# Optimization experiments

Measured on AMD Instinct MI355X. Metric: run time of the kernel, lower is better.

The kernel has to match this reference:

```python
import jax, jax.numpy as jnp
import numpy as np

B = 64
E = 512          # latent_size / h_dim
H = 8            # num_heads
D = E // H       # head_dim
MAX_AGENTS = 254 # max(agents_per_sample) for the deterministic counts below
NEG = -1e9


def setup_inputs() -> dict:
    key = jax.random.key(0)
    k_x, k_wi, k_bi, k_wo, k_bo = jax.random.split(key, 5)
    # deterministic variable agent counts in [128, 254]; sum == 11531, max == 254
    agents = jnp.array([128 + (3 * i) % 129 for i in range(B)], dtype=jnp.int32)
    total = 11531
    att_in = jax.random.normal(k_x, (total, E), dtype=jnp.float32)
    # nn.MultiheadAttention params: packed in-proj [3E, E] + bias, out-proj [E, E] + bias
    w_in = jax.random.normal(k_wi, (3 * E, E), dtype=jnp.float32) * 0.02
    b_in = jax.random.normal(k_bi, (3 * E,), dtype=jnp.float32) * 0.02
    w_out = jax.random.normal(k_wo, (E, E), dtype=jnp.float32) * 0.02
    b_out = jax.random.normal(k_bo, (E,), dtype=jnp.float32) * 0.02
    return {"att_in": att_in, "w_in": w_in, "b_in": b_in,
            "w_out": w_out, "b_out": b_out, "agents_per_sample": agents}


def reference(att_in, w_in, b_in, w_out, b_out, agents_per_sample):
    S = MAX_AGENTS
    # scatter packed rows into padded [B, S, E] via a clipped gather (jit-safe)
    offsets = jnp.cumsum(agents_per_sample) - agents_per_sample      # [B]
    pos = jnp.arange(S, dtype=jnp.int32)
    mask = pos[None, :] < agents_per_sample[:, None]                 # [B, S] valid
    idx = jnp.clip(offsets[:, None] + pos[None, :], 0, att_in.shape[0] - 1)
    padded = jnp.where(mask[..., None], att_in[idx], 0.0)            # [B, S, E]

    # fused QKV projection (torch packed in_proj), dropout disabled (eval)
    qkv = padded @ w_in.T + b_in                                     # [B, S, 3E]
    q, k, v = jnp.split(qkv, 3, axis=-1)
    q = q.reshape(B, S, H, D)
    k = k.reshape(B, S, H, D)
    v = v.reshape(B, S, H, D)

    scores = jnp.einsum('bqhd,bkhd->bhqk', q, k) * (D ** -0.5)      # [B, H, S, S]
    scores = jnp.where(mask[:, None, None, :], scores, NEG)          # key_padding_mask
    attn = jax.nn.softmax(scores, axis=-1)
    ctx = jnp.einsum('bhqk,bkhd->bqhd', attn, v).reshape(B, S, E)
    out = ctx @ w_out.T + b_out                                      # [B, S, E]
    # torch returns only valid rows per sample; zero the padded rows instead
    return out * mask[..., None]
```

## Files before the change

kernel.cpp:

```cpp
#include <hip/hip_runtime.h>
#include <hip/hip_bf16.h>

typedef __attribute__((ext_vector_type(8))) short bf16x8;
typedef __attribute__((ext_vector_type(4))) float f32x4;
typedef __attribute__((ext_vector_type(4))) int i32x4;
typedef __attribute__((ext_vector_type(4))) unsigned short u16x4;
typedef __attribute__((ext_vector_type(2))) unsigned ui2;
typedef __attribute__((ext_vector_type(4))) float fl4;

struct __attribute__((packed)) u16x4u { u16x4 v; };

__device__ __forceinline__ f32x4 mfma16(bf16x8 a, bf16x8 b, f32x4 c) {
    return __builtin_amdgcn_mfma_f32_16x16x32_bf16(a, b, c, 0, 0, 0);
}

__device__ __forceinline__ unsigned short f2b(float f) {
    unsigned u = __float_as_uint(f);
    unsigned r = (u + 0x7FFF + ((u >> 16) & 1)) >> 16;
    return (unsigned short)r;
}

__device__ __forceinline__ int bsearch_off(const int* s_off, int m) {
    int lo = 0, hi = 63;
    while (lo < hi) {
        int mid = (lo + hi + 1) >> 1;
        if (s_off[mid] <= m) lo = mid; else hi = mid - 1;
    }
    return lo;
}

__device__ __forceinline__ void gld_lds16(const __hip_bfloat16* g, __hip_bfloat16* l) {
    __builtin_amdgcn_global_load_lds(
        (const __attribute__((address_space(1))) void*)g,
        (__attribute__((address_space(3))) void*)l,
        16, 0, 0);
}

__global__ void k_prep(const unsigned short* __restrict__ src,
                       const void* __restrict__ b_in, const void* __restrict__ b_out,
                       const int* __restrict__ agents,
                       int* __restrict__ flag, int* __restrict__ offs,
                       float* __restrict__ bfi, float* __restrict__ bfo) {
    __shared__ int sh[256];
    __shared__ int sa[64];
    __shared__ int sflag;
    int tid = threadIdx.x;
    int h = 0;
    for (int i = tid; i < 16384; i += 256) {
        unsigned e = (src[i] >> 7) & 0xFF;
        if (e == 0xFF) h = 1;
    }
    sh[tid] = h;
    if (tid < 64) sa[tid] = agents[tid];
    __syncthreads();
    if (tid < 64) {
        int v = sh[tid] | sh[tid + 64] | sh[tid + 128] | sh[tid + 192];
        unsigned long long m = __ballot(v != 0);
        if (tid == 0) { flag[0] = (m != 0) ? 1 : 0; sflag = (m != 0) ? 1 : 0; }
        int ex = 0;
        for (int i = 0; i < 64; ++i) { int w = sa[i]; if (i < tid) ex += w; }
        offs[tid] = ex;
        if (tid == 63) offs[64] = ex + sa[63];
    }
    __syncthreads();
    int f = sflag;
    for (int i = tid; i < 1536; i += 256)
        bfi[i] = f ? ((const float*)b_in)[i]
                   : __bfloat162float(((const __hip_bfloat16*)b_in)[i]);
    for (int i = tid; i < 512; i += 256)
        bfo[i] = f ? ((const float*)b_out)[i]
                   : __bfloat162float(((const __hip_bfloat16*)b_out)[i]);
}

__global__ void k_cast_all(const void* __restrict__ sA, unsigned short* __restrict__ dA, int nA,
                           const void* __restrict__ sWi, unsigned short* __restrict__ dWi, int nWi,
                           const void* __restrict__ sWo, unsigned short* __restrict__ dWo, int nWo,
                           const int* __restrict__ flag) {
    int i = (blockIdx.x * 256 + threadIdx.x) * 4;
    const void* src; unsigned short* dst; int k;
    if (i < nA)            { src = sA;  dst = dA;  k = i; }
    else if (i < nA + nWi) { src = sWi; dst = dWi; k = i - nA; }
    else if (i < nA + nWi + nWo) { src = sWo; dst = dWo; k = i - nA - nWi; }
    else return;
    u16x4 o;
    if (flag[0]) {
        fl4 v = *(const fl4*)((const float*)src + k);
        o[0] = f2b(v[0]); o[1] = f2b(v[1]); o[2] = f2b(v[2]); o[3] = f2b(v[3]);
    } else {
        o = *(const u16x4*)((const unsigned short*)src + k);
    }
    *(u16x4*)(dst + k) = o;
}

template<int LDA, bool MROWS>
__device__ __forceinline__ void gemm_core(
    const __hip_bfloat16* __restrict__ A,
    const __hip_bfloat16* __restrict__ W,
    int m0, int n0, int total,
    __hip_bfloat16* As, __hip_bfloat16* Ws,
    f32x4 acc[4][2], int tid)
{
    int lane = tid & 63, quad = lane >> 4, c = lane & 15;
    int wave = tid >> 6;
    int wm = wave >> 2, wn = wave & 3;

    const __hip_bfloat16* gA[2];
    const __hip_bfloat16* gW[2];
    __hip_bfloat16* lA[2];
    __hip_bfloat16* lW[2];
#pragma unroll
    for (int j = 0; j < 2; ++j) {
        int L = j * 512 + tid;
        int row = L >> 3;
        int gseg = (L & 7) ^ (row & 7);
        int ar = m0 + row; if (ar > total - 1) ar = total - 1;
        gA[j] = A + (size_t)ar * LDA + gseg * 8;
        gW[j] = W + (size_t)(n0 + row) * 512 + gseg * 8;
        lA[j] = As + (size_t)(j * 512 + wave * 64) * 8;
        lW[j] = Ws + (size_t)(j * 512 + wave * 64) * 8;
    }

#pragma unroll
    for (int j = 0; j < 2; ++j) gld_lds16(gA[j], lA[j]);
#pragma unroll
    for (int j = 0; j < 2; ++j) gld_lds16(gW[j], lW[j]);

#pragma unroll
    for (int s = 0; s < 8; ++s) {
        const int cur = s & 1;
        const int nxt = cur ^ 1;
        if (s < 7) {
            int k0 = (s + 1) * 64;
#pragma unroll
            for (int j = 0; j < 2; ++j) gld_lds16(gA[j] + k0, lA[j] + nxt * (128 * 64));
#pragma unroll
            for (int j = 0; j < 2; ++j) gld_lds16(gW[j] + k0, lW[j] + nxt * (128 * 64));
            asm volatile("s_waitcnt vmcnt(4)" ::: "memory");
        } else {
            asm volatile("s_waitcnt vmcnt(0)" ::: "memory");
        }
        __builtin_amdgcn_s_barrier();
        const __hip_bfloat16* Ab = As + cur * (128 * 64);
        const __hip_bfloat16* Wb = Ws + cur * (128 * 64);
#pragma unroll
        for (int h = 0; h < 2; ++h) {
            bf16x8 af[4], wf[2];
            int ks = quad + 4 * h;
#pragma unroll
            for (int t = 0; t < 4; ++t) {
                int rowa = wm * 64 + t * 16 + c;
                af[t] = *(const bf16x8*)(Ab + (size_t)rowa * 64 + ((ks ^ (rowa & 7)) * 8));
            }
#pragma unroll
            for (int t = 0; t < 2; ++t) {
                int rowb = wn * 32 + t * 16 + c;
                wf[t] = *(const bf16x8*)(Wb + (size_t)rowb * 64 + ((ks ^ (rowb & 7)) * 8));
            }
#pragma unroll
            for (int i = 0; i < 4; ++i)
#pragma unroll
                for (int j = 0; j < 2; ++j)
                    acc[i][j] = MROWS ? mfma16(af[i], wf[j], acc[i][j])
                                      : mfma16(wf[j], af[i], acc[i][j]);
        }
        if (s < 7) __builtin_amdgcn_s_barrier();
    }
}

__global__ __launch_bounds__(512, 4) void k_qkv(
    const __hip_bfloat16* __restrict__ A,
    const __hip_bfloat16* __restrict__ W,
    const float* __restrict__ bias,
    const int* __restrict__ offs,
    __hip_bfloat16* __restrict__ qP,
    __hip_bfloat16* __restrict__ kP,
    __hip_bfloat16* __restrict__ vT,
    int total, int MT)
{
    __shared__ __hip_bfloat16 As[2 * 128 * 64];
    __shared__ __hip_bfloat16 Ws[2 * 128 * 64];
    __shared__ int s_off[65];
    int l = blockIdx.x;
    int inner = l >> 3;
    int cb = inner % 12;
    int rb = (l & 7) + 8 * (inner / 12);
    if (rb >= MT) return;
    int n0 = cb * 128;
    int m0 = rb * 128;
    int tid = threadIdx.x;
    if (tid < 65) s_off[tid] = offs[tid];
    int lane = tid & 63, quad = lane >> 4, c = lane & 15;
    int wave = tid >> 6, wm = wave >> 2, wn = wave & 3;
    f32x4 z = {0.f, 0.f, 0.f, 0.f};
    f32x4 acc[4][2] = {{z,z},{z,z},{z,z},{z,z}};

    if (n0 < 1024) {
        gemm_core<512, false>(A, W, m0, n0, total, As, Ws, acc, tid);
        __hip_bfloat16* dst = (n0 < 512) ? qP : kP;
        int nb = n0 & 511;
        int head = (nb + wn * 32) >> 6;
        int cb32 = (wn & 1) * 32;
        fl4 bv4[2];
#pragma unroll
        for (int j = 0; j < 2; ++j)
            bv4[j] = *(const fl4*)&bias[n0 + wn * 32 + j * 16 + quad * 4];
#pragma unroll
        for (int i = 0; i < 4; ++i) {
            int m = m0 + wm * 64 + i * 16 + c;
            if (m >= total) continue;
            int lo = bsearch_off(s_off, m);
            int vs = m - s_off[lo];
            size_t rowp = ((size_t)(lo * 8 + head) * 256 + vs) * 64;
#pragma unroll
            for (int j = 0; j < 2; ++j) {
                int dcol = cb32 + j * 16 + quad * 4;
                u16x4 o;
#pragma unroll
                for (int r = 0; r < 4; ++r) o[r] = f2b(acc[i][j][r] + bv4[j][r]);
                *(u16x4*)&dst[rowp + dcol] = o;
            }
        }
    } else {
        gemm_core<512, true>(A, W, m0, n0, total, As, Ws, acc, tid);
        float bv[2];
#pragma unroll
        for (int j = 0; j < 2; ++j) bv[j] = bias[n0 + wn * 32 + j * 16 + c];
#pragma unroll
        for (int i = 0; i < 4; ++i) {
            int m_base = m0 + wm * 64 + i * 16 + quad * 4;
            if (m_base >= total) continue;
            int lo = bsearch_off(s_off, m_base);
            bool vec = (m_base + 3 < total) && (s_off[lo + 1] > m_base + 3);
            if (vec) {
                int vs = m_base - s_off[lo];
#pragma unroll
                for (int j = 0; j < 2; ++j) {
                    int vc = n0 - 1024 + wn * 32 + j * 16 + c;
                    size_t idx = ((size_t)(lo * 8 + (vc >> 6)) * 64 + (vc & 63)) * 256 + vs;
                    u16x4 o;
#pragma unroll
                    for (int r = 0; r < 4; ++r) o[r] = f2b(acc[i][j][r] + bv[j]);
                    ((u16x4u*)&vT[idx])->v = o;
                }
            } else {
#pragma unroll
                for (int r = 0; r < 4; ++r) {
                    int m = m_base + r;
                    if (m >= total) continue;
                    int lo2 = bsearch_off(s_off, m);
                    int vs2 = m - s_off[lo2];
#pragma unroll
                    for (int j = 0; j < 2; ++j) {
                        int vc = n0 - 1024 + wn * 32 + j * 16 + c;
                        vT[((size_t)(lo2 * 8 + (vc >> 6)) * 64 + (vc & 63)) * 256 + vs2] =
                            __float2bfloat16(acc[i][j][r] + bv[j]);
                    }
                }
            }
        }
    }
}

__global__ __launch_bounds__(256, 2) void k_attn(
    const __hip_bfloat16* __restrict__ qP,
    const __hip_bfloat16* __restrict__ kP,
    const __hip_bfloat16* __restrict__ vT,
    __hip_bfloat16* __restrict__ ctx,
    const int* __restrict__ agents,
    const int* __restrict__ offs)
{
    __shared__ __attribute__((aligned(16))) char Pl[4][16 * 80];
    int bh = blockIdx.x;
    int b = bh >> 3, h = bh & 7;
    int n = agents[b];
    int off = offs[b];
    int qtiles = (n + 15) >> 4;
    int stmax = (qtiles + 1) >> 1;
    int tid = threadIdx.x;
    int wave = tid >> 6, lane = tid & 63, quad = lane >> 4, c = lane & 15;
    const __hip_bfloat16* qbase = qP + (size_t)bh * 256 * 64;
    const __hip_bfloat16* kbase = kP + (size_t)bh * 256 * 64 + quad * 8;
    const __hip_bfloat16* vbase = vT + (size_t)bh * 64 * 256;
    char* Plw = &Pl[wave][0];

    bf16x8 qB[4][2];
    int nt = 0;
#pragma unroll
    for (int t = 0; t < 4; ++t) {
        int qt = wave + 4 * t;
        if (qt < qtiles) {
            nt = t + 1;
            int qr = qt * 16 + c; if (qr > n - 1) qr = n - 1;
            const __hip_bfloat16* qp = qbase + (size_t)qr * 64 + quad * 8;
            qB[t][0] = *(const bf16x8*)qp;
            qB[t][1] = *(const bf16x8*)(qp + 32);
        }
    }

    f32x4 z = {0.f, 0.f, 0.f, 0.f};
    f32x4 O[4][4] = {{z,z,z,z},{z,z,z,z},{z,z,z,z},{z,z,z,z}};
    float sm[4] = {0.f, 0.f, 0.f, 0.f};

    auto LK = [&](int st, bf16x8 kA[2][2], bf16x8 vA[4]) {
        int k0 = st * 32;
#pragma unroll
        for (int ti = 0; ti < 2; ++ti) {
            int kr = k0 + ti * 16 + c; if (kr > n - 1) kr = n - 1;
            const __hip_bfloat16* kp = kbase + (size_t)kr * 64;
            kA[ti][0] = *(const bf16x8*)kp;
            kA[ti][1] = *(const bf16x8*)(kp + 32);
        }
#pragma unroll
        for (int dt = 0; dt < 4; ++dt)
            vA[dt] = *(const bf16x8*)(vbase + (size_t)(dt * 16 + c) * 256 + k0 + quad * 8);
    };

    auto CMP = [&](int st, bf16x8 kA[2][2], bf16x8 vA[4]) {
        int k0 = st * 32;
#pragma unroll
        for (int t = 0; t < 4; ++t) {
            if (t < nt) {
#pragma unroll
                for (int ti = 0; ti < 2; ++ti) {
                    f32x4 s = mfma16(kA[ti][0], qB[t][0], z);
                    s = mfma16(kA[ti][1], qB[t][1], s);
                    int kbase_i = k0 + ti * 16 + quad * 4;
                    float p0 = (kbase_i + 0 < n) ? __expf(s[0] * 0.125f) : 0.f;
                    float p1 = (kbase_i + 1 < n) ? __expf(s[1] * 0.125f) : 0.f;
                    float p2 = (kbase_i + 2 < n) ? __expf(s[2] * 0.125f) : 0.f;
                    float p3 = (kbase_i + 3 < n) ? __expf(s[3] * 0.125f) : 0.f;
                    sm[t] += (p0 + p1) + (p2 + p3);
                    ui2 dw;
                    dw[0] = (unsigned)f2b(p0) | ((unsigned)f2b(p1) << 16);
                    dw[1] = (unsigned)f2b(p2) | ((unsigned)f2b(p3) << 16);
                    *(ui2*)(Plw + c * 80 + ti * 32 + quad * 8) = dw;
                }
                bf16x8 pB = *(const bf16x8*)(Plw + c * 80 + quad * 16);
#pragma unroll
                for (int dt = 0; dt < 4; ++dt)
                    O[t][dt] = mfma16(vA[dt], pB, O[t][dt]);
            }
        }
    };

    bf16x8 kA[2][2], vA[4], kB[2][2], vB[4], kC[2][2], vC[4];
    LK(0, kA, vA);
    if (1 < stmax) LK(1, kB, vB);
    for (int st = 0; st < stmax; st += 3) {
        if (st + 2 < stmax) LK(st + 2, kC, vC);
        CMP(st, kA, vA);
        if (st + 3 < stmax) LK(st + 3, kA, vA);
        if (st + 1 < stmax) CMP(st + 1, kB, vB);
        if (st + 4 < stmax) LK(st + 4, kB, vB);
        if (st + 2 < stmax) CMP(st + 2, kC, vC);
    }

#pragma unroll
    for (int t = 0; t < 4; ++t) {
        if (t < nt) {
            float v = sm[t];
            v += __shfl_xor(v, 16);
            v += __shfl_xor(v, 32);
            float iv = 1.0f / v;
            int q = (wave + 4 * t) * 16 + c;
            if (q < n) {
                size_t row = (size_t)(off + q) * 512 + h * 64;
#pragma unroll
                for (int dt = 0; dt < 4; ++dt) {
                    u16x4 o;
#pragma unroll
                    for (int r = 0; r < 4; ++r) o[r] = f2b(O[t][dt][r] * iv);
                    *(u16x4*)&ctx[row + dt * 16 + quad * 4] = o;
                }
            }
        }
    }
}

__global__ __launch_bounds__(512, 4) void k_out(
    const __hip_bfloat16* __restrict__ A,
    const __hip_bfloat16* __restrict__ W,
    const float* __restrict__ bias,
    const int* __restrict__ offs,
    const int* __restrict__ agents,
    void* __restrict__ out,
    const int* __restrict__ flag,
    int total, int MT)
{
    __shared__ __hip_bfloat16 As[2 * 128 * 64];
    __shared__ __hip_bfloat16 Ws[2 * 128 * 64];
    __shared__ int s_off[65];
    int l = blockIdx.x;
    int MTpad = ((MT + 7) >> 3) << 3;
    int tid = threadIdx.x;
    if (l >= 4 * MTpad) {
        int b = l - 4 * MTpad;
        int n = agents[b];
        int esz = flag[0] ? 4 : 2;
        long long base = ((long long)b * 254 + n) * 512 * esz;
        long long bytes = (long long)(254 - n) * 512 * esz;
        for (long long i = (long long)tid * 16; i < bytes; i += (long long)512 * 16)
            *(i32x4*)((char*)out + base + i) = (i32x4){0, 0, 0, 0};
        return;
    }
    int inner = l >> 3;
    int cb = inner & 3;
    int rb = (l & 7) + 8 * (inner >> 2);
    if (rb >= MT) return;
    int n0 = cb * 128;
    int m0 = rb * 128;
    if (tid < 65) s_off[tid] = offs[tid];
    f32x4 z = {0.f, 0.f, 0.f, 0.f};
    f32x4 acc[4][2] = {{z,z},{z,z},{z,z},{z,z}};
    gemm_core<512, false>(A, W, m0, n0, total, As, Ws, acc, tid);

    int f32m = flag[0];
    int lane = tid & 63, quad = lane >> 4, c = lane & 15;
    int wave = tid >> 6, wm = wave >> 2, wn = wave & 3;
    fl4 bv4[2];
#pragma unroll
    for (int j = 0; j < 2; ++j)
        bv4[j] = *(const fl4*)&bias[n0 + wn * 32 + j * 16 + quad * 4];
#pragma unroll
    for (int i = 0; i < 4; ++i) {
        int m = m0 + wm * 64 + i * 16 + c;
        if (m >= total) continue;
        int lo = bsearch_off(s_off, m);
        int os_ = m - s_off[lo];
        size_t rowb = ((size_t)(lo * 254 + os_)) * 512;
#pragma unroll
        for (int j = 0; j < 2; ++j) {
            int col0 = n0 + wn * 32 + j * 16 + quad * 4;
            if (f32m) {
                fl4 o;
#pragma unroll
                for (int r = 0; r < 4; ++r) o[r] = acc[i][j][r] + bv4[j][r];
                *(fl4*)&((float*)out)[rowb + col0] = o;
            } else {
                u16x4 o;
#pragma unroll
                for (int r = 0; r < 4; ++r) o[r] = f2b(acc[i][j][r] + bv4[j][r]);
                *(u16x4*)&((__hip_bfloat16*)out)[rowb + col0] = o;
            }
        }
    }
}

extern "C" void kernel_launch(void* const* d_in, const int* in_sizes, int n_in,
                              void* d_out, int out_size, void* d_ws, size_t ws_size,
                              hipStream_t stream) {
    const void* att_in = d_in[0];
    const void* w_in   = d_in[1];
    const void* b_in   = d_in[2];
    const void* w_out  = d_in[3];
    const void* b_out  = d_in[4];
    const int* agents  = (const int*)d_in[5];
    int total = in_sizes[0] / 512;

    char* p = (char*)d_ws;
    int* flag  = (int*)p;                 p += 256;
    int* offs  = (int*)p;                 p += 512;
    float* bfi = (float*)p;               p += 1536 * 4;
    float* bfo = (float*)p;               p += 512 * 4;
    __hip_bfloat16* WinBf  = (__hip_bfloat16*)p;  p += (size_t)1536 * 512 * 2;
    __hip_bfloat16* WoutBf = (__hip_bfloat16*)p;  p += (size_t)512 * 512 * 2;
    __hip_bfloat16* Abf    = (__hip_bfloat16*)p;  p += (size_t)total * 512 * 2;
    __hip_bfloat16* qP     = (__hip_bfloat16*)p;  p += (size_t)512 * 256 * 64 * 2;
    __hip_bfloat16* kP     = (__hip_bfloat16*)p;  p += (size_t)512 * 256 * 64 * 2;
    __hip_bfloat16* vT     = (__hip_bfloat16*)p;  p += (size_t)512 * 64 * 256 * 2;
    __hip_bfloat16* ctx    = (__hip_bfloat16*)p;  p += (size_t)total * 512 * 2;

    int nA = total * 512, nWi = 1536 * 512, nWo = 512 * 512;
    int ntot = nA + nWi + nWo;

    k_prep<<<1, 256, 0, stream>>>((const unsigned short*)att_in, b_in, b_out,
                                  agents, flag, offs, bfi, bfo);
    k_cast_all<<<(ntot / 4 + 255) / 256, 256, 0, stream>>>(
        att_in, (unsigned short*)Abf, nA,
        w_in,   (unsigned short*)WinBf, nWi,
        w_out,  (unsigned short*)WoutBf, nWo, flag);

    int MT = (total + 127) / 128;
    int MTpad = ((MT + 7) / 8) * 8;
    k_qkv<<<12 * MTpad, 512, 0, stream>>>(Abf, WinBf, bfi, offs, qP, kP, vT, total, MT);
    k_attn<<<512, 256, 0, stream>>>(qP, kP, vT, ctx, agents, offs);
    k_out<<<4 * MTpad + 64, 512, 0, stream>>>(ctx, WoutBf, bfo, offs, agents,
                                              d_out, flag, total, MT);
}
```

Before: 173.4 us.

## Triple-buffer A tiles in GEMM core and reuse LDS for segment offsets

The shared GEMM core now keeps three LDS buffers for A tiles and two for W tiles, so A loads are issued two k-steps ahead and more global loads stay in flight, with the waitcnt thresholds changed to match. The offsets table no longer has its own shared array. It is loaded into the A buffer after the GEMM, behind extra barriers. The extra 16 KB of A buffer raises LDS use per block and may reduce how many blocks fit on a CU.

Measured after the change: 175.1 us. About the same (+1.0%).

```diff
diff --git a/kernel.cpp b/kernel.cpp
--- a/kernel.cpp
+++ b/kernel.cpp
@@ -97,7 +97,8 @@
     const __hip_bfloat16* __restrict__ A,
     const __hip_bfloat16* __restrict__ W,
     int m0, int n0, int total,
-    __hip_bfloat16* As, __hip_bfloat16* Ws,
+    __hip_bfloat16* As,
+    __hip_bfloat16* Ws,
     f32x4 acc[4][2], int tid)
 {
     int lane = tid & 63, quad = lane >> 4, c = lane & 15;
@@ -124,24 +125,32 @@
     for (int j = 0; j < 2; ++j) gld_lds16(gA[j], lA[j]);
 #pragma unroll
     for (int j = 0; j < 2; ++j) gld_lds16(gW[j], lW[j]);
+#pragma unroll
+    for (int j = 0; j < 2; ++j) gld_lds16(gA[j] + 64, lA[j] + 8192);
 
 #pragma unroll
     for (int s = 0; s < 8; ++s) {
-        const int cur = s & 1;
-        const int nxt = cur ^ 1;
-        if (s < 7) {
-            int k0 = (s + 1) * 64;
-#pragma unroll
-            for (int j = 0; j < 2; ++j) gld_lds16(gA[j] + k0, lA[j] + nxt * (128 * 64));
-#pragma unroll
-            for (int j = 0; j < 2; ++j) gld_lds16(gW[j] + k0, lW[j] + nxt * (128 * 64));
+        const int curA = s % 3;
+        const int curW = s & 1;
+        if (s < 6) {
+#pragma unroll
+            for (int j = 0; j < 2; ++j)
+                gld_lds16(gW[j] + (s + 1) * 64, lW[j] + ((s + 1) & 1) * 8192);
+#pragma unroll
+            for (int j = 0; j < 2; ++j)
+                gld_lds16(gA[j] + (s + 2) * 64, lA[j] + ((s + 2) % 3) * 8192);
+            asm volatile("s_waitcnt vmcnt(6)" ::: "memory");
+        } else if (s == 6) {
+#pragma unroll
+            for (int j = 0; j < 2; ++j)
+                gld_lds16(gW[j] + 7 * 64, lW[j] + 8192);
             asm volatile("s_waitcnt vmcnt(4)" ::: "memory");
         } else {
             asm volatile("s_waitcnt vmcnt(0)" ::: "memory");
         }
         __builtin_amdgcn_s_barrier();
-        const __hip_bfloat16* Ab = As + cur * (128 * 64);
-        const __hip_bfloat16* Wb = Ws + cur * (128 * 64);
+        const __hip_bfloat16* Ab = As + curA * 8192;
+        const __hip_bfloat16* Wb = Ws + curW * 8192;
 #pragma unroll
         for (int h = 0; h < 2; ++h) {
             bf16x8 af[4], wf[2];
@@ -177,9 +186,8 @@
     __hip_bfloat16* __restrict__ vT,
     int total, int MT)
 {
-    __shared__ __hip_bfloat16 As[2 * 128 * 64];
+    __shared__ __hip_bfloat16 As[3 * 128 * 64];
     __shared__ __hip_bfloat16 Ws[2 * 128 * 64];
-    __shared__ int s_off[65];
     int l = blockIdx.x;
     int inner = l >> 3;
     int cb = inner % 12;
@@ -188,7 +196,6 @@
     int n0 = cb * 128;
     int m0 = rb * 128;
     int tid = threadIdx.x;
-    if (tid < 65) s_off[tid] = offs[tid];
     int lane = tid & 63, quad = lane >> 4, c = lane & 15;
     int wave = tid >> 6, wm = wave >> 2, wn = wave & 3;
     f32x4 z = {0.f, 0.f, 0.f, 0.f};
@@ -196,6 +203,10 @@
 
     if (n0 < 1024) {
         gemm_core<512, false>(A, W, m0, n0, total, As, Ws, acc, tid);
+        __syncthreads();
+        if (tid < 65) ((int*)As)[tid] = offs[tid];
+        __syncthreads();
+        const int* s_off = (const int*)As;
         __hip_bfloat16* dst = (n0 < 512) ? qP : kP;
         int nb = n0 & 511;
         int head = (nb + wn * 32) >> 6;
@@ -222,6 +233,10 @@
         }
     } else {
         gemm_core<512, true>(A, W, m0, n0, total, As, Ws, acc, tid);
+        __syncthreads();
+        if (tid < 65) ((int*)As)[tid] = offs[tid];
+        __syncthreads();
+        const int* s_off = (const int*)As;
         float bv[2];
 #pragma unroll
         for (int j = 0; j < 2; ++j) bv[j] = bias[n0 + wn * 32 + j * 16 + c];
@@ -387,9 +402,8 @@
     const int* __restrict__ flag,
     int total, int MT)
 {
-    __shared__ __hip_bfloat16 As[2 * 128 * 64];
+    __shared__ __hip_bfloat16 As[3 * 128 * 64];
     __shared__ __hip_bfloat16 Ws[2 * 128 * 64];
-    __shared__ int s_off[65];
     int l = blockIdx.x;
     int MTpad = ((MT + 7) >> 3) << 3;
     int tid = threadIdx.x;
@@ -409,10 +423,13 @@
     if (rb >= MT) return;
     int n0 = cb * 128;
     int m0 = rb * 128;
-    if (tid < 65) s_off[tid] = offs[tid];
     f32x4 z = {0.f, 0.f, 0.f, 0.f};
     f32x4 acc[4][2] = {{z,z},{z,z},{z,z},{z,z}};
     gemm_core<512, false>(A, W, m0, n0, total, As, Ws, acc, tid);
+    __syncthreads();
+    if (tid < 65) ((int*)As)[tid] = offs[tid];
+    __syncthreads();
+    const int* s_off = (const int*)As;
 
     int f32m = flag[0];
     int lane = tid & 63, quad = lane >> 4, c = lane & 15;
```
